# Optimization experiments

Measured on AMD Instinct MI355X. Metric: run time of the kernel, lower is better.

## Reference

```python
import jax, jax.numpy as jnp
import numpy as np

N_NODES = 50000
N_EDGES = 600000
N_FEAT = 128
N_GRAPHS = 256
DIM = 95
N_OUT = 12
N_ITER = 10
BN_EPS = 1e-5


def setup_inputs() -> dict:
    key = jax.random.key(0)
    ks = jax.random.split(key, 16)
    inp = {}
    inp["x"] = jax.random.normal(ks[0], (N_NODES, N_FEAT), dtype=jnp.float32)
    inp["edge_index"] = jax.random.randint(ks[1], (2, N_EDGES), 0, N_NODES, dtype=jnp.int64)
    inp["batch"] = jnp.sort(jax.random.randint(ks[2], (N_NODES,), 0, N_GRAPHS, dtype=jnp.int64))
    def lin(k, fan_in, fan_out):
        bound = 1.0 / np.sqrt(fan_in)
        kw, kb = jax.random.split(k)
        W = jax.random.uniform(kw, (fan_in, fan_out), jnp.float32, -bound, bound)
        b = jax.random.uniform(kb, (fan_out,), jnp.float32, -bound, bound)
        return W, b
    inp["W1a"], inp["b1a"] = lin(ks[3], N_FEAT, N_FEAT)            # nn1 layer 1
    inp["W1b"], inp["b1b"] = lin(ks[4], N_FEAT, N_FEAT)            # nn1 layer 2
    inp["gamma"] = jnp.ones((N_FEAT,), jnp.float32)                 # bn1 weight
    inp["beta"] = jnp.zeros((N_FEAT,), jnp.float32)                 # bn1 bias
    inp["Wl1"], inp["bl1"] = lin(ks[5], 2 * N_FEAT, N_FEAT // 2)   # lin1
    inp["Wl2"], inp["bl2"] = lin(ks[6], 2 * N_FEAT, N_FEAT // 2)   # lin2
    inp["Wm1"], inp["bm1"] = lin(ks[7], N_FEAT, DIM)               # MLP layer 1
    inp["Wm2"], inp["bm2"] = lin(ks[8], DIM, N_OUT)                # MLP layer 2
    return inp


def reference(x, edge_index, batch, W1a, b1a, W1b, b1b, gamma, beta,
              Wl1, bl1, Wl2, bl2, Wm1, bm1, Wm2, bm2):
    src, dst = edge_index[0], edge_index[1]
    # GINConv (eps=0): h_i = nn1(x_i + sum_{j->i} x_j)
    agg = jax.ops.segment_sum(x[src], dst, num_segments=N_NODES)
    h0 = x + agg
    h0 = jax.nn.relu(h0 @ W1a + b1a) @ W1b + b1b
    x1 = jax.nn.relu(h0)
    # BatchNorm1d (training mode: batch statistics, biased variance)
    mean = jnp.mean(x1, axis=0)
    var = jnp.mean(jnp.square(x1 - mean), axis=0)
    x1 = gamma * (x1 - mean) * jax.lax.rsqrt(var + BN_EPS) + beta
    # global_mean_pool over graph ids
    sums = jax.ops.segment_sum(x1, batch, num_segments=N_GRAPHS)
    counts = jax.ops.segment_sum(jnp.ones((N_NODES,), x1.dtype), batch, num_segments=N_GRAPHS)
    xg = sums / jnp.maximum(counts, 1.0)[:, None]
    # recurrent gated loop
    h = xg
    for _ in range(N_ITER):
        cat = jnp.concatenate([xg, h], axis=1)          # [G, 2*F]
        p = cat @ Wl1 + bl1
        q = cat @ Wl2 + bl2
        h = jnp.concatenate([jnp.tanh(q), jax.nn.sigmoid(p)], axis=1)
    # output MLP
    return jax.nn.relu(h @ Wm1 + bm1) @ Wm2 + bm2
```

## Files before the change

### kernel.cpp

```cpp
#include <hip/hip_runtime.h>
#include <cstddef>

#define N_NODES  50000
#define N_EDGES  600000
#define N_FEAT   128
#define N_GRAPHS 256
#define DIMM     95
#define N_OUTD   12
#define N_ITERS  10

#define N_CHUNKS 196

#define WS_STATS 0
#define WS_XG    (WS_STATS + 256)
#define WS_CNT   (WS_XG + N_GRAPHS * N_FEAT)
#define WS_OFF   (WS_CNT + N_NODES)
#define WS_CUR   (WS_OFF + N_NODES + 4)
#define WS_CHS   (WS_CUR + N_NODES)
#define WS_SORT  (WS_CHS + 256)

#define SR 132
#define TR 48

__global__ void k_zero(float* __restrict__ ws) {
    int i = blockIdx.x * 256 + threadIdx.x;
    int* cnt = (int*)ws + WS_CNT;
    if (i < N_NODES) cnt[i] = 0;
    if (i < 256) ws[WS_STATS + i] = 0.f;
    if (i < N_GRAPHS * N_FEAT) ws[WS_XG + i] = 0.f;
}

__global__ void k_hist(const int* __restrict__ ei, float* __restrict__ ws) {
    int e = blockIdx.x * 256 + threadIdx.x;
    int* cnt = (int*)ws + WS_CNT;
    if (e < N_EDGES) atomicAdd(&cnt[ei[N_EDGES + e]], 1);
}

__global__ void k_chunk(float* __restrict__ ws) {
    __shared__ int red[4];
    const int tid = threadIdx.x;
    int* cnt = (int*)ws + WS_CNT;
    int i = blockIdx.x * 256 + tid;
    int v = (i < N_NODES) ? cnt[i] : 0;
    #pragma unroll
    for (int d = 32; d; d >>= 1) v += __shfl_down(v, d);
    if ((tid & 63) == 0) red[tid >> 6] = v;
    __syncthreads();
    if (tid == 0) ((int*)ws + WS_CHS)[blockIdx.x] = red[0] + red[1] + red[2] + red[3];
}

__global__ void k_scan0(float* __restrict__ ws) {
    __shared__ int s[256];
    const int tid = threadIdx.x;
    int* chs = (int*)ws + WS_CHS;
    int v = (tid < N_CHUNKS) ? chs[tid] : 0;
    s[tid] = v;
    __syncthreads();
    #pragma unroll
    for (int d = 1; d < 256; d <<= 1) {
        int t = (tid >= d) ? s[tid - d] : 0;
        __syncthreads();
        s[tid] += t;
        __syncthreads();
    }
    if (tid < N_CHUNKS) chs[tid] = s[tid] - v;
    if (tid == 0) ((int*)ws + WS_OFF)[N_NODES] = N_EDGES;
}

__global__ void k_scan1(float* __restrict__ ws) {
    __shared__ int s[256];
    const int tid = threadIdx.x;
    int* cnt = (int*)ws + WS_CNT;
    int* off = (int*)ws + WS_OFF;
    int* cur = (int*)ws + WS_CUR;
    int i = blockIdx.x * 256 + tid;
    int v = (i < N_NODES) ? cnt[i] : 0;
    s[tid] = v;
    __syncthreads();
    #pragma unroll
    for (int d = 1; d < 256; d <<= 1) {
        int t = (tid >= d) ? s[tid - d] : 0;
        __syncthreads();
        s[tid] += t;
        __syncthreads();
    }
    int o = ((int*)ws + WS_CHS)[blockIdx.x] + s[tid] - v;
    if (i < N_NODES) { off[i] = o; cur[i] = o; }
}

__global__ void k_scatter(const int* __restrict__ ei, float* __restrict__ ws) {
    int e = blockIdx.x * 256 + threadIdx.x;
    if (e >= N_EDGES) return;
    int d = ei[N_EDGES + e];
    int s = ei[e];
    int* cur = (int*)ws + WS_CUR;
    int pos = atomicAdd(&cur[d], 1);
    ((int*)ws + WS_SORT)[pos] = s;
}

__global__ __launch_bounds__(256, 4) void k_fused(const float* __restrict__ x,
        const int* __restrict__ batch, float* __restrict__ ws,
        const float* __restrict__ W1a, const float* __restrict__ b1a,
        const float* __restrict__ W1b, const float* __restrict__ b1b) {
    __shared__ float As[TR * SR];
    __shared__ float red[256];
    __shared__ int batch_l[TR];
    const int tid  = threadIdx.x;
    const int lane = tid & 63;
    const int wv   = tid >> 6;
    const int fg   = tid & 15;
    const int rg   = tid >> 4;
    const int row0 = blockIdx.x * TR;

    const int* off = (const int*)ws + WS_OFF;
    const int* ss  = (const int*)ws + WS_SORT;
    const float2* __restrict__ x2 = (const float2*)x;

    if (tid < TR) {
        int r = row0 + tid;
        batch_l[tid] = (r < N_NODES) ? batch[r] : (N_GRAPHS - 1);
    }

    for (int ii = 0; ii < 12; ii += 4) {
        int lo[4], deg[4], idxv[4];
        float2 acc[4];
        #pragma unroll
        for (int t = 0; t < 4; ++t) {
            const int r = row0 + wv * 12 + ii + t;
            const bool valid = r < N_NODES;
            lo[t] = valid ? off[r] : 0;
            int hi = valid ? off[r + 1] : 0;
            deg[t] = hi - lo[t];
            acc[t] = valid ? x2[(size_t)r * 64 + lane] : make_float2(0.f, 0.f);
            idxv[t] = (lane < min(deg[t], 64)) ? ss[lo[t] + lane] : 0;
        }
        const int dmax = min(max(max(deg[0], deg[1]), max(deg[2], deg[3])), 64);
        for (int j = 0; j < dmax; j += 2) {
            float2 v[8];
            #pragma unroll
            for (int t = 0; t < 4; ++t) {
                if (j < deg[t]) {
                    int s = __shfl(idxv[t], j);
                    v[t] = x2[(size_t)s * 64 + lane];
                } else v[t] = make_float2(0.f, 0.f);
            }
            #pragma unroll
            for (int t = 0; t < 4; ++t) {
                if (j + 1 < deg[t]) {
                    int s = __shfl(idxv[t], j + 1);
                    v[4 + t] = x2[(size_t)s * 64 + lane];
                } else v[4 + t] = make_float2(0.f, 0.f);
            }
            #pragma unroll
            for (int t = 0; t < 4; ++t) {
                acc[t].x += v[t].x + v[4 + t].x;
                acc[t].y += v[t].y + v[4 + t].y;
            }
        }
        #pragma unroll
        for (int t = 0; t < 4; ++t) {
            if (deg[t] > 64) {
                for (int c0 = lo[t] + 64; c0 < lo[t] + deg[t]; c0 += 64) {
                    const int cd = min(64, lo[t] + deg[t] - c0);
                    int mi = (lane < cd) ? ss[c0 + lane] : 0;
                    for (int j = 0; j < cd; ++j) {
                        int s = __shfl(mi, j);
                        float2 vv = x2[(size_t)s * 64 + lane];
                        acc[t].x += vv.x; acc[t].y += vv.y;
                    }
                }
            }
        }
        #pragma unroll
        for (int t = 0; t < 4; ++t)
            *(float2*)(As + (wv * 12 + ii + t) * SR + 2 * lane) = acc[t];
    }
    __syncthreads();

    float acc[3][8];
    #pragma unroll
    for (int i = 0; i < 3; ++i)
        #pragma unroll
        for (int j = 0; j < 8; ++j) acc[i][j] = 0.f;

    #pragma unroll 2
    for (int k = 0; k < N_FEAT; k += 4) {
        float4 w[8];
        #pragma unroll
        for (int kk = 0; kk < 4; ++kk) {
            w[2 * kk]     = *(const float4*)(W1a + (k + kk) * N_FEAT + fg * 8);
            w[2 * kk + 1] = *(const float4*)(W1a + (k + kk) * N_FEAT + fg * 8 + 4);
        }
        #pragma unroll
        for (int i = 0; i < 3; ++i) {
            const float4 a4 = *(const float4*)(As + (rg * 3 + i) * SR + k);
            const float av[4] = {a4.x, a4.y, a4.z, a4.w};
            #pragma unroll
            for (int kk = 0; kk < 4; ++kk) {
                acc[i][0] += av[kk] * w[2 * kk].x;
                acc[i][1] += av[kk] * w[2 * kk].y;
                acc[i][2] += av[kk] * w[2 * kk].z;
                acc[i][3] += av[kk] * w[2 * kk].w;
                acc[i][4] += av[kk] * w[2 * kk + 1].x;
                acc[i][5] += av[kk] * w[2 * kk + 1].y;
                acc[i][6] += av[kk] * w[2 * kk + 1].z;
                acc[i][7] += av[kk] * w[2 * kk + 1].w;
            }
        }
    }
    __syncthreads();

    {
        const float4 ba0 = *(const float4*)(b1a + fg * 8);
        const float4 ba1 = *(const float4*)(b1a + fg * 8 + 4);
        #pragma unroll
        for (int i = 0; i < 3; ++i) {
            float4 u0, u1;
            u0.x = fmaxf(acc[i][0] + ba0.x, 0.f); u0.y = fmaxf(acc[i][1] + ba0.y, 0.f);
            u0.z = fmaxf(acc[i][2] + ba0.z, 0.f); u0.w = fmaxf(acc[i][3] + ba0.w, 0.f);
            u1.x = fmaxf(acc[i][4] + ba1.x, 0.f); u1.y = fmaxf(acc[i][5] + ba1.y, 0.f);
            u1.z = fmaxf(acc[i][6] + ba1.z, 0.f); u1.w = fmaxf(acc[i][7] + ba1.w, 0.f);
            *(float4*)(As + (rg * 3 + i) * SR + fg * 8)     = u0;
            *(float4*)(As + (rg * 3 + i) * SR + fg * 8 + 4) = u1;
        }
    }
    __syncthreads();

    #pragma unroll
    for (int i = 0; i < 3; ++i)
        #pragma unroll
        for (int j = 0; j < 8; ++j) acc[i][j] = 0.f;

    #pragma unroll 2
    for (int k = 0; k < N_FEAT; k += 4) {
        float4 w[8];
        #pragma unroll
        for (int kk = 0; kk < 4; ++kk) {
            w[2 * kk]     = *(const float4*)(W1b + (k + kk) * N_FEAT + fg * 8);
            w[2 * kk + 1] = *(const float4*)(W1b + (k + kk) * N_FEAT + fg * 8 + 4);
        }
        #pragma unroll
        for (int i = 0; i < 3; ++i) {
            const float4 a4 = *(const float4*)(As + (rg * 3 + i) * SR + k);
            const float av[4] = {a4.x, a4.y, a4.z, a4.w};
            #pragma unroll
            for (int kk = 0; kk < 4; ++kk) {
                acc[i][0] += av[kk] * w[2 * kk].x;
                acc[i][1] += av[kk] * w[2 * kk].y;
                acc[i][2] += av[kk] * w[2 * kk].z;
                acc[i][3] += av[kk] * w[2 * kk].w;
                acc[i][4] += av[kk] * w[2 * kk + 1].x;
                acc[i][5] += av[kk] * w[2 * kk + 1].y;
                acc[i][6] += av[kk] * w[2 * kk + 1].z;
                acc[i][7] += av[kk] * w[2 * kk + 1].w;
            }
        }
    }
    __syncthreads();

    {
        const float4 bb0 = *(const float4*)(b1b + fg * 8);
        const float4 bb1 = *(const float4*)(b1b + fg * 8 + 4);
        #pragma unroll
        for (int i = 0; i < 3; ++i) {
            float4 u0, u1;
            u0.x = fmaxf(acc[i][0] + bb0.x, 0.f); u0.y = fmaxf(acc[i][1] + bb0.y, 0.f);
            u0.z = fmaxf(acc[i][2] + bb0.z, 0.f); u0.w = fmaxf(acc[i][3] + bb0.w, 0.f);
            u1.x = fmaxf(acc[i][4] + bb1.x, 0.f); u1.y = fmaxf(acc[i][5] + bb1.y, 0.f);
            u1.z = fmaxf(acc[i][6] + bb1.z, 0.f); u1.w = fmaxf(acc[i][7] + bb1.w, 0.f);
            *(float4*)(As + (rg * 3 + i) * SR + fg * 8)     = u0;
            *(float4*)(As + (rg * 3 + i) * SR + fg * 8 + 4) = u1;
        }
    }
    __syncthreads();

    {
        const int c = tid & 127;
        const int h = tid >> 7;
        float sum = 0.f, sq = 0.f, pool = 0.f;
        int curg = batch_l[h * 24];
        bool any = (row0 + h * 24) < N_NODES;
        #pragma unroll 4
        for (int rr = 0; rr < 24; ++rr) {
            int rl = h * 24 + rr;
            if (row0 + rl >= N_NODES) break;
            float v = As[rl * SR + c];
            int g = batch_l[rl];
            if (g != curg) {
                unsafeAtomicAdd(ws + WS_XG + (size_t)curg * N_FEAT + c, pool);
                pool = 0.f; curg = g;
            }
            sum += v; sq += v * v; pool += v;
        }
        if (any) unsafeAtomicAdd(ws + WS_XG + (size_t)curg * N_FEAT + c, pool);
        if (h == 1) { red[c] = sum; red[128 + c] = sq; }
        __syncthreads();
        if (h == 0) {
            unsafeAtomicAdd(ws + WS_STATS + c, sum + red[c]);
            unsafeAtomicAdd(ws + WS_STATS + 128 + c, sq + red[128 + c]);
        }
    }
}

__device__ __forceinline__ int lbound(const int* __restrict__ a, int n, int v) {
    int lo = 0, hi = n;
    while (lo < hi) { int m = (lo + hi) >> 1; if (a[m] < v) lo = m + 1; else hi = m; }
    return lo;
}

__global__ __launch_bounds__(256) void k_recur(const float* __restrict__ ws,
        const int* __restrict__ batch,
        const float* __restrict__ gamma, const float* __restrict__ beta,
        const float* __restrict__ Wl1, const float* __restrict__ bl1,
        const float* __restrict__ Wl2, const float* __restrict__ bl2,
        const float* __restrict__ Wm1, const float* __restrict__ bm1,
        const float* __restrict__ Wm2, const float* __restrict__ bm2,
        float* __restrict__ out) {
    __shared__ float W1h[128 * 64];
    __shared__ float W2h[128 * 64];
    __shared__ float xg_s[128];
    __shared__ float h_s[128];
    __shared__ float px[2][64];
    __shared__ float pq[2][2][64];
    __shared__ float m_s[DIMM];
    __shared__ int range[2];
    const int g = blockIdx.x, tid = threadIdx.x;

    if (tid < 2) range[tid] = lbound(batch, N_NODES, g + tid);
    for (int i = tid; i < 128 * 64; i += 256) {
        W1h[i] = Wl1[128 * 64 + i];
        W2h[i] = Wl2[128 * 64 + i];
    }
    __syncthreads();
    if (tid < 128) {
        const int cnt = range[1] - range[0];
        float mean = ws[WS_STATS + tid] * (1.f / N_NODES);
        float var  = fmaxf(ws[WS_STATS + 128 + tid] * (1.f / N_NODES) - mean * mean, 0.f);
        float sc = gamma[tid] * rsqrtf(var + 1e-5f);
        float sh = beta[tid] - mean * sc;
        float pool = ws[WS_XG + (size_t)g * N_FEAT + tid];
        float v = (cnt > 0) ? (sc * pool / (float)cnt + sh) : 0.f;
        xg_s[tid] = v;
        h_s[tid] = v;
    }
    __syncthreads();

    const int sel  = tid >> 7;
    const int part = (tid >> 6) & 1;
    const int j    = tid & 63;

    {
        const float* Wg = sel ? Wl2 : Wl1;
        float a = 0.f;
        const int k0 = part * 64;
        #pragma unroll 4
        for (int k = 0; k < 64; ++k) a += xg_s[k0 + k] * Wg[(k0 + k) * 64 + j];
        pq[sel][part][j] = a;
    }
    __syncthreads();
    if (part == 0) {
        const float* bias = sel ? bl2 : bl1;
        px[sel][j] = pq[sel][0][j] + pq[sel][1][j] + bias[j];
    }
    __syncthreads();

    const float* Wh = sel ? W2h : W1h;
    for (int it = 0; it < N_ITERS; ++it) {
        float a = 0.f;
        const int k0 = part * 64;
        #pragma unroll
        for (int k = 0; k < 64; k += 4) {
            const float4 h4 = *(const float4*)(h_s + k0 + k);
            a += h4.x * Wh[(k0 + k + 0) * 64 + j];
            a += h4.y * Wh[(k0 + k + 1) * 64 + j];
            a += h4.z * Wh[(k0 + k + 2) * 64 + j];
            a += h4.w * Wh[(k0 + k + 3) * 64 + j];
        }
        pq[sel][part][j] = a;
        __syncthreads();
        if (part == 0) {
            float tot = pq[sel][0][j] + pq[sel][1][j] + px[sel][j];
            if (sel == 0) h_s[64 + j] = 1.f / (1.f + expf(-tot));
            else          h_s[j] = tanhf(tot);
        }
        __syncthreads();
    }

    if (tid < DIMM) {
        float a = bm1[tid];
        #pragma unroll 4
        for (int k = 0; k < 128; ++k) a += h_s[k] * Wm1[k * DIMM + tid];
        m_s[tid] = fmaxf(a, 0.f);
    }
    __syncthreads();
    if (tid < N_OUTD) {
        float a = bm2[tid];
        for (int k = 0; k < DIMM; ++k) a += m_s[k] * Wm2[k * N_OUTD + tid];
        out[g * N_OUTD + tid] = a;
    }
}

extern "C" void kernel_launch(void* const* d_in, const int* in_sizes, int n_in,
                              void* d_out, int out_size, void* d_ws, size_t ws_size,
                              hipStream_t stream) {
    const float* x     = (const float*)d_in[0];
    const int*   ei    = (const int*)d_in[1];
    const int*   batch = (const int*)d_in[2];
    const float* W1a = (const float*)d_in[3];
    const float* b1a = (const float*)d_in[4];
    const float* W1b = (const float*)d_in[5];
    const float* b1b = (const float*)d_in[6];
    const float* gamma = (const float*)d_in[7];
    const float* beta  = (const float*)d_in[8];
    const float* Wl1 = (const float*)d_in[9];
    const float* bl1 = (const float*)d_in[10];
    const float* Wl2 = (const float*)d_in[11];
    const float* bl2 = (const float*)d_in[12];
    const float* Wm1 = (const float*)d_in[13];
    const float* bm1 = (const float*)d_in[14];
    const float* Wm2 = (const float*)d_in[15];
    const float* bm2 = (const float*)d_in[16];
    float* out = (float*)d_out;
    float* ws  = (float*)d_ws;

    k_zero   <<<(N_NODES + 255) / 256, 256, 0, stream>>>(ws);
    k_hist   <<<(N_EDGES + 255) / 256, 256, 0, stream>>>(ei, ws);
    k_chunk  <<<N_CHUNKS, 256, 0, stream>>>(ws);
    k_scan0  <<<1, 256, 0, stream>>>(ws);
    k_scan1  <<<N_CHUNKS, 256, 0, stream>>>(ws);
    k_scatter<<<(N_EDGES + 255) / 256, 256, 0, stream>>>(ei, ws);
    k_fused  <<<(N_NODES + TR - 1) / TR, 256, 0, stream>>>(x, batch, ws, W1a, b1a, W1b, b1b);
    k_recur  <<<N_GRAPHS, 256, 0, stream>>>(ws, batch, gamma, beta,
                                            Wl1, bl1, Wl2, bl2, Wm1, bm1, Wm2, bm2, out);
}
```

Before: 313.5 us.

## Merge CSR build into cooperative kernel and gather neighbors from fp16 copy

Replaces the six small CSR-construction kernels with one cooperative kernel that uses grid syncs between phases, removing several launch gaps. The same kernel also writes an fp16 copy of x, and the edge aggregation in the fused kernel now gathers neighbour rows from that copy, halving gather bytes while accumulating in fp32. This costs an extra pass that converts x and introduces fp16 rounding into the aggregated features. The scatter and histogram phases now run on only 256 blocks using grid-stride loops, which may reduce parallelism for the atomics.

Measured after the change: 486.0 us. 1.55x slower.

```diff
diff --git a/kernel.cpp b/kernel.cpp
--- a/kernel.cpp
+++ b/kernel.cpp
@@ -1,5 +1,9 @@
 #include <hip/hip_runtime.h>
+#include <hip/hip_fp16.h>
+#include <hip/hip_cooperative_groups.h>
 #include <cstddef>
+
+namespace cg = cooperative_groups;
 
 #define N_NODES  50000
 #define N_EDGES  600000
@@ -18,84 +22,92 @@
 #define WS_CUR   (WS_OFF + N_NODES + 4)
 #define WS_CHS   (WS_CUR + N_NODES)
 #define WS_SORT  (WS_CHS + 256)
+#define WS_XH    (WS_SORT + N_EDGES)
 
 #define SR 132
 #define TR 48
 
-__global__ void k_zero(float* __restrict__ ws) {
-    int i = blockIdx.x * 256 + threadIdx.x;
-    int* cnt = (int*)ws + WS_CNT;
-    if (i < N_NODES) cnt[i] = 0;
-    if (i < 256) ws[WS_STATS + i] = 0.f;
-    if (i < N_GRAPHS * N_FEAT) ws[WS_XG + i] = 0.f;
-}
-
-__global__ void k_hist(const int* __restrict__ ei, float* __restrict__ ws) {
-    int e = blockIdx.x * 256 + threadIdx.x;
-    int* cnt = (int*)ws + WS_CNT;
-    if (e < N_EDGES) atomicAdd(&cnt[ei[N_EDGES + e]], 1);
-}
-
-__global__ void k_chunk(float* __restrict__ ws) {
+__global__ __launch_bounds__(256) void k_build(const int* __restrict__ ei,
+                                               const float* __restrict__ x,
+                                               float* __restrict__ ws) {
+    cg::grid_group grid = cg::this_grid();
+    __shared__ int s[256];
     __shared__ int red[4];
-    const int tid = threadIdx.x;
-    int* cnt = (int*)ws + WS_CNT;
-    int i = blockIdx.x * 256 + tid;
-    int v = (i < N_NODES) ? cnt[i] : 0;
-    #pragma unroll
-    for (int d = 32; d; d >>= 1) v += __shfl_down(v, d);
-    if ((tid & 63) == 0) red[tid >> 6] = v;
-    __syncthreads();
-    if (tid == 0) ((int*)ws + WS_CHS)[blockIdx.x] = red[0] + red[1] + red[2] + red[3];
-}
-
-__global__ void k_scan0(float* __restrict__ ws) {
-    __shared__ int s[256];
-    const int tid = threadIdx.x;
-    int* chs = (int*)ws + WS_CHS;
-    int v = (tid < N_CHUNKS) ? chs[tid] : 0;
-    s[tid] = v;
-    __syncthreads();
-    #pragma unroll
-    for (int d = 1; d < 256; d <<= 1) {
-        int t = (tid >= d) ? s[tid - d] : 0;
-        __syncthreads();
-        s[tid] += t;
-        __syncthreads();
-    }
-    if (tid < N_CHUNKS) chs[tid] = s[tid] - v;
-    if (tid == 0) ((int*)ws + WS_OFF)[N_NODES] = N_EDGES;
-}
-
-__global__ void k_scan1(float* __restrict__ ws) {
-    __shared__ int s[256];
-    const int tid = threadIdx.x;
+    const int tid  = threadIdx.x;
+    const int gtid = blockIdx.x * 256 + tid;
+    const int nthr = gridDim.x * 256;
+
     int* cnt = (int*)ws + WS_CNT;
     int* off = (int*)ws + WS_OFF;
     int* cur = (int*)ws + WS_CUR;
-    int i = blockIdx.x * 256 + tid;
-    int v = (i < N_NODES) ? cnt[i] : 0;
-    s[tid] = v;
-    __syncthreads();
-    #pragma unroll
-    for (int d = 1; d < 256; d <<= 1) {
-        int t = (tid >= d) ? s[tid - d] : 0;
-        __syncthreads();
-        s[tid] += t;
-        __syncthreads();
-    }
-    int o = ((int*)ws + WS_CHS)[blockIdx.x] + s[tid] - v;
-    if (i < N_NODES) { off[i] = o; cur[i] = o; }
-}
-
-__global__ void k_scatter(const int* __restrict__ ei, float* __restrict__ ws) {
-    int e = blockIdx.x * 256 + threadIdx.x;
-    if (e >= N_EDGES) return;
-    int d = ei[N_EDGES + e];
-    int s = ei[e];
-    int* cur = (int*)ws + WS_CUR;
-    int pos = atomicAdd(&cur[d], 1);
-    ((int*)ws + WS_SORT)[pos] = s;
+    int* chs = (int*)ws + WS_CHS;
+    int* srt = (int*)ws + WS_SORT;
+
+    for (int i = gtid; i < N_NODES; i += nthr) cnt[i] = 0;
+    if (gtid < 256) ws[WS_STATS + gtid] = 0.f;
+    for (int i = gtid; i < N_GRAPHS * N_FEAT; i += nthr) ws[WS_XG + i] = 0.f;
+    {
+        const float2* __restrict__ x2 = (const float2*)x;
+        __half2* __restrict__ xh2 = (__half2*)(ws + WS_XH);
+        for (int i = gtid; i < N_NODES * 64; i += nthr)
+            xh2[i] = __float22half2_rn(x2[i]);
+    }
+    grid.sync();
+
+    for (int e = gtid; e < N_EDGES; e += nthr)
+        atomicAdd(&cnt[ei[N_EDGES + e]], 1);
+    grid.sync();
+
+    if (blockIdx.x < N_CHUNKS) {
+        int i = blockIdx.x * 256 + tid;
+        int v = (i < N_NODES) ? cnt[i] : 0;
+        #pragma unroll
+        for (int d = 32; d; d >>= 1) v += __shfl_down(v, d);
+        if ((tid & 63) == 0) red[tid >> 6] = v;
+        __syncthreads();
+        if (tid == 0) chs[blockIdx.x] = red[0] + red[1] + red[2] + red[3];
+    }
+    grid.sync();
+
+    if (blockIdx.x == 0) {
+        int v = (tid < N_CHUNKS) ? chs[tid] : 0;
+        s[tid] = v;
+        __syncthreads();
+        #pragma unroll
+        for (int d = 1; d < 256; d <<= 1) {
+            int t = (tid >= d) ? s[tid - d] : 0;
+            __syncthreads();
+            s[tid] += t;
+            __syncthreads();
+        }
+        if (tid < N_CHUNKS) chs[tid] = s[tid] - v;
+        if (tid == 0) off[N_NODES] = N_EDGES;
+    }
+    grid.sync();
+
+    if (blockIdx.x < N_CHUNKS) {
+        int i = blockIdx.x * 256 + tid;
+        int v = (i < N_NODES) ? cnt[i] : 0;
+        s[tid] = v;
+        __syncthreads();
+        #pragma unroll
+        for (int d = 1; d < 256; d <<= 1) {
+            int t = (tid >= d) ? s[tid - d] : 0;
+            __syncthreads();
+            s[tid] += t;
+            __syncthreads();
+        }
+        int o = chs[blockIdx.x] + s[tid] - v;
+        if (i < N_NODES) { off[i] = o; cur[i] = o; }
+    }
+    grid.sync();
+
+    for (int e = gtid; e < N_EDGES; e += nthr) {
+        int d  = ei[N_EDGES + e];
+        int sc = ei[e];
+        int pos = atomicAdd(&cur[d], 1);
+        srt[pos] = sc;
+    }
 }
 
 __global__ __launch_bounds__(256, 4) void k_fused(const float* __restrict__ x,
@@ -115,6 +127,7 @@
     const int* off = (const int*)ws + WS_OFF;
     const int* ss  = (const int*)ws + WS_SORT;
     const float2* __restrict__ x2 = (const float2*)x;
+    const __half2* __restrict__ xh2 = (const __half2*)(ws + WS_XH);
 
     if (tid < TR) {
         int r = row0 + tid;
@@ -136,25 +149,27 @@
         }
         const int dmax = min(max(max(deg[0], deg[1]), max(deg[2], deg[3])), 64);
         for (int j = 0; j < dmax; j += 2) {
-            float2 v[8];
+            __half2 v[8];
             #pragma unroll
             for (int t = 0; t < 4; ++t) {
                 if (j < deg[t]) {
                     int s = __shfl(idxv[t], j);
-                    v[t] = x2[(size_t)s * 64 + lane];
-                } else v[t] = make_float2(0.f, 0.f);
+                    v[t] = xh2[(size_t)s * 64 + lane];
+                } else v[t] = __half2half2(__float2half(0.f));
             }
             #pragma unroll
             for (int t = 0; t < 4; ++t) {
                 if (j + 1 < deg[t]) {
                     int s = __shfl(idxv[t], j + 1);
-                    v[4 + t] = x2[(size_t)s * 64 + lane];
-                } else v[4 + t] = make_float2(0.f, 0.f);
+                    v[4 + t] = xh2[(size_t)s * 64 + lane];
+                } else v[4 + t] = __half2half2(__float2half(0.f));
             }
             #pragma unroll
             for (int t = 0; t < 4; ++t) {
-                acc[t].x += v[t].x + v[4 + t].x;
-                acc[t].y += v[t].y + v[4 + t].y;
+                float2 f0 = __half22float2(v[t]);
+                float2 f1 = __half22float2(v[4 + t]);
+                acc[t].x += f0.x + f1.x;
+                acc[t].y += f0.y + f1.y;
             }
         }
         #pragma unroll
@@ -165,7 +180,7 @@
                     int mi = (lane < cd) ? ss[c0 + lane] : 0;
                     for (int j = 0; j < cd; ++j) {
                         int s = __shfl(mi, j);
-                        float2 vv = x2[(size_t)s * 64 + lane];
+                        float2 vv = __half22float2(xh2[(size_t)s * 64 + lane]);
                         acc[t].x += vv.x; acc[t].y += vv.y;
                     }
                 }
@@ -423,13 +438,11 @@
     float* out = (float*)d_out;
     float* ws  = (float*)d_ws;
 
-    k_zero   <<<(N_NODES + 255) / 256, 256, 0, stream>>>(ws);
-    k_hist   <<<(N_EDGES + 255) / 256, 256, 0, stream>>>(ei, ws);
-    k_chunk  <<<N_CHUNKS, 256, 0, stream>>>(ws);
-    k_scan0  <<<1, 256, 0, stream>>>(ws);
-    k_scan1  <<<N_CHUNKS, 256, 0, stream>>>(ws);
-    k_scatter<<<(N_EDGES + 255) / 256, 256, 0, stream>>>(ei, ws);
-    k_fused  <<<(N_NODES + TR - 1) / TR, 256, 0, stream>>>(x, batch, ws, W1a, b1a, W1b, b1b);
-    k_recur  <<<N_GRAPHS, 256, 0, stream>>>(ws, batch, gamma, beta,
-                                            Wl1, bl1, Wl2, bl2, Wm1, bm1, Wm2, bm2, out);
+    {
+        void* args[] = {(void*)&ei, (void*)&x, (void*)&ws};
+        hipLaunchCooperativeKernel((void*)k_build, dim3(256), dim3(256), args, 0, stream);
+    }
+    k_fused<<<(N_NODES + TR - 1) / TR, 256, 0, stream>>>(x, batch, ws, W1a, b1a, W1b, b1b);
+    k_recur<<<N_GRAPHS, 256, 0, stream>>>(ws, batch, gamma, beta,
+                                          Wl1, bl1, Wl2, bl2, Wm1, bm1, Wm2, bm2, out);
 }
```

## Gather neighbor rows with float4 half-wave lanes and vectorize weight staging

Applied to the files above, without the earlier changes.

The GIN aggregation gather now splits each wavefront into two 32-lane halves, each handling a different node and loading 16-byte float4 chunks per lane instead of float2. Neighbor indices are fetched in 32-wide chunks, and a single loop replaces the separate overflow path for degree above 64. The aim is fewer, wider memory transactions and better latency hiding per gathered row. The pooled-MLP kernel also copies the Wl1/Wl2 halves into shared memory with unrolled float4 loads. The change adds some divergence when the two nodes sharing a wavefront have different degrees.

Result: no change. 312.3 us (-0.4%).

```diff
diff --git a/kernel.cpp b/kernel.cpp
--- a/kernel.cpp
+++ b/kernel.cpp
@@ -108,13 +108,15 @@
     const int tid  = threadIdx.x;
     const int lane = tid & 63;
     const int wv   = tid >> 6;
+    const int half = lane >> 5;
+    const int sl   = lane & 31;
     const int fg   = tid & 15;
     const int rg   = tid >> 4;
     const int row0 = blockIdx.x * TR;
 
     const int* off = (const int*)ws + WS_OFF;
     const int* ss  = (const int*)ws + WS_SORT;
-    const float2* __restrict__ x2 = (const float2*)x;
+    const float4* __restrict__ x4 = (const float4*)x;
 
     if (tid < TR) {
         int r = row0 + tid;
@@ -122,58 +124,55 @@
     }
 
     for (int ii = 0; ii < 12; ii += 4) {
-        int lo[4], deg[4], idxv[4];
-        float2 acc[4];
-        #pragma unroll
-        for (int t = 0; t < 4; ++t) {
-            const int r = row0 + wv * 12 + ii + t;
+        float4 acc[2];
+        int lo[2], deg[2];
+        int need = 0;
+        #pragma unroll
+        for (int p = 0; p < 2; ++p) {
+            const int rl = wv * 12 + ii + 2 * p + half;
+            const int r  = row0 + rl;
             const bool valid = r < N_NODES;
-            lo[t] = valid ? off[r] : 0;
-            int hi = valid ? off[r + 1] : 0;
-            deg[t] = hi - lo[t];
-            acc[t] = valid ? x2[(size_t)r * 64 + lane] : make_float2(0.f, 0.f);
-            idxv[t] = (lane < min(deg[t], 64)) ? ss[lo[t] + lane] : 0;
-        }
-        const int dmax = min(max(max(deg[0], deg[1]), max(deg[2], deg[3])), 64);
-        for (int j = 0; j < dmax; j += 2) {
-            float2 v[8];
+            lo[p]  = valid ? off[r] : 0;
+            int hi = valid ? off[r + 1] : lo[p];
+            deg[p] = hi - lo[p];
+            acc[p] = valid ? x4[(size_t)r * 32 + sl] : make_float4(0.f, 0.f, 0.f, 0.f);
+            int dmx = max(deg[p], __shfl_xor(deg[p], 32));
+            need = max(need, dmx);
+        }
+        for (int c0 = 0; c0 < need; c0 += 32) {
+            int idxp[2];
             #pragma unroll
-            for (int t = 0; t < 4; ++t) {
-                if (j < deg[t]) {
-                    int s = __shfl(idxv[t], j);
-                    v[t] = x2[(size_t)s * 64 + lane];
-                } else v[t] = make_float2(0.f, 0.f);
-            }
-            #pragma unroll
-            for (int t = 0; t < 4; ++t) {
-                if (j + 1 < deg[t]) {
-                    int s = __shfl(idxv[t], j + 1);
-                    v[4 + t] = x2[(size_t)s * 64 + lane];
-                } else v[4 + t] = make_float2(0.f, 0.f);
-            }
-            #pragma unroll
-            for (int t = 0; t < 4; ++t) {
-                acc[t].x += v[t].x + v[4 + t].x;
-                acc[t].y += v[t].y + v[4 + t].y;
-            }
-        }
-        #pragma unroll
-        for (int t = 0; t < 4; ++t) {
-            if (deg[t] > 64) {
-                for (int c0 = lo[t] + 64; c0 < lo[t] + deg[t]; c0 += 64) {
-                    const int cd = min(64, lo[t] + deg[t] - c0);
-                    int mi = (lane < cd) ? ss[c0 + lane] : 0;
-                    for (int j = 0; j < cd; ++j) {
-                        int s = __shfl(mi, j);
-                        float2 vv = x2[(size_t)s * 64 + lane];
-                        acc[t].x += vv.x; acc[t].y += vv.y;
-                    }
+            for (int p = 0; p < 2; ++p)
+                idxp[p] = (c0 + sl < deg[p]) ? ss[lo[p] + c0 + sl] : 0;
+            const int dmc = min(32, need - c0);
+            for (int j = 0; j < dmc; j += 2) {
+                float4 v[4];
+                #pragma unroll
+                for (int p = 0; p < 2; ++p) {
+                    int s0 = __shfl(idxp[p], (half << 5) + j);
+                    v[p] = (c0 + j < deg[p]) ? x4[(size_t)s0 * 32 + sl]
+                                             : make_float4(0.f, 0.f, 0.f, 0.f);
+                }
+                #pragma unroll
+                for (int p = 0; p < 2; ++p) {
+                    int s1 = __shfl(idxp[p], (half << 5) + j + 1);
+                    v[2 + p] = (c0 + j + 1 < deg[p]) ? x4[(size_t)s1 * 32 + sl]
+                                                     : make_float4(0.f, 0.f, 0.f, 0.f);
+                }
+                #pragma unroll
+                for (int p = 0; p < 2; ++p) {
+                    acc[p].x += v[p].x + v[2 + p].x;
+                    acc[p].y += v[p].y + v[2 + p].y;
+                    acc[p].z += v[p].z + v[2 + p].z;
+                    acc[p].w += v[p].w + v[2 + p].w;
                 }
             }
         }
         #pragma unroll
-        for (int t = 0; t < 4; ++t)
-            *(float2*)(As + (wv * 12 + ii + t) * SR + 2 * lane) = acc[t];
+        for (int p = 0; p < 2; ++p) {
+            const int rl = wv * 12 + ii + 2 * p + half;
+            *(float4*)(As + rl * SR + 4 * sl) = acc[p];
+        }
     }
     __syncthreads();
 
@@ -327,9 +326,16 @@
     const int g = blockIdx.x, tid = threadIdx.x;
 
     if (tid < 2) range[tid] = lbound(batch, N_NODES, g + tid);
-    for (int i = tid; i < 128 * 64; i += 256) {
-        W1h[i] = Wl1[128 * 64 + i];
-        W2h[i] = Wl2[128 * 64 + i];
+    {
+        const float4* w1 = (const float4*)(Wl1 + 128 * 64);
+        const float4* w2 = (const float4*)(Wl2 + 128 * 64);
+        float4* d1 = (float4*)W1h;
+        float4* d2 = (float4*)W2h;
+        #pragma unroll
+        for (int i = 0; i < 8; ++i) {
+            d1[tid + i * 256] = w1[tid + i * 256];
+            d2[tid + i * 256] = w2[tid + i * 256];
+        }
     }
     __syncthreads();
     if (tid < 128) {
```
